# Optimization experiments

Measured on AMD Instinct MI355X. Metric: run time of the kernel, lower is better.

The kernel has to match this reference:

```python
import jax, jax.numpy as jnp
import numpy as np

B, S, D = 8, 2048, 2048
A, L = 4, 256  # audio placeholders per type per sequence, codes per placeholder
IN_IDX, OUT_IDX, PAD_ID, IGNORE = 128011, 128012, 128001, -100


def setup_inputs() -> dict:
    key = jax.random.key(0)
    k1, k2, k3, k4, k5 = jax.random.split(key, 5)
    ids = np.asarray(jax.random.randint(k1, (B, S), 0, 32000, dtype=jnp.int32)).copy()
    ids[:, np.array([100, 500, 900, 1300])] = IN_IDX
    ids[:, np.array([1700, 1800, 1900, 2000])] = OUT_IDX
    n_in = n_out = B * A
    # merged length: same for every row -> no left-pad shift, no column trim
    max_token_num = S - 2 * A + 2 * A * L  # 4088, multiple of round_to=8
    return {
        "audio_in_embed": jax.random.normal(k2, (n_in * L, D), jnp.float32),
        "audio_out_embed": jax.random.normal(k3, (n_out * L, D), jnp.float32),
        "inputs_embeds": jax.random.normal(k4, (B, S, D), jnp.float32),
        "audio_in_ids_start": jnp.arange(n_in, dtype=jnp.int32) * L,
        "audio_out_ids_start": jnp.arange(n_out, dtype=jnp.int32) * L,
        "input_ids": jnp.asarray(ids, jnp.int32),
        "attention_mask": jnp.ones((B, S), jnp.int32),
        "label_ids": jax.random.randint(k5, (B, S), 0, 32000, dtype=jnp.int32),
        "max_token_num": int(max_token_num),
        "n_in": int(n_in),
        "n_out": int(n_out),
        "n_text": int(B * S - 2 * B * A),
    }


def _codes_length(starts, total):
    # torch: concat([starts[1:]-starts[:-1], [total - starts[-1]]])
    return jnp.concatenate([starts[1:], jnp.array([total], starts.dtype)]) - starts


def _merge(audio_in_embed, audio_out_embed, inputs_embeds, audio_in_ids_start,
           audio_out_ids_start, input_ids, attention_mask, label_ids,
           max_token_num, n_in, n_out, n_text):
    Bb, Ss = input_ids.shape
    Dd = inputs_embeds.shape[-1]
    M = max_token_num

    in_mask = input_ids == IN_IDX
    out_mask = input_ids == OUT_IDX
    text_mask = ~(in_mask | out_mask)

    in_len = _codes_length(audio_in_ids_start, audio_in_embed.shape[0])
    out_len = _codes_length(audio_out_ids_start, audio_out_embed.shape[0])

    # row-major placeholder positions (matches torch.where ordering)
    bi_in, si_in = jnp.nonzero(in_mask, size=n_in)
    bi_out, si_out = jnp.nonzero(out_mask, size=n_out)
    bt, st = jnp.nonzero(text_mask, size=n_text)

    tpn = jnp.ones((Bb, Ss), jnp.int32)
    tpn = tpn.at[bi_in, si_in].set(in_len).at[bi_out, si_out].set(out_len)
    new_pos = jnp.cumsum(tpn, axis=-1) - 1
    new_pos = new_pos + (M - 1 - new_pos[:, -1])[:, None]  # left padding shift

    final_embedding = jnp.zeros((Bb, M, Dd), inputs_embeds.dtype)
    final_attention = jnp.zeros((Bb, M), attention_mask.dtype)
    final_input_ids = jnp.full((Bb, M), PAD_ID, input_ids.dtype)
    final_labels = jnp.full((Bb, M), IGNORE, label_ids.dtype)
    in_fill = jnp.zeros((Bb, M), bool)
    out_fill = jnp.zeros((Bb, M), bool)

    def fill(embed, starts, lens, b_idx, s_idx, tok_idx, FE, FI, FL, FM):
        # map each embed row -> (batch, merged column) in one gather/scatter
        r = jnp.arange(embed.shape[0], dtype=starts.dtype)
        p = jnp.searchsorted(starts, r, side='right') - 1  # placeholder id per row
        ends = new_pos[b_idx, s_idx]                        # last merged col per placeholder
        cols = ends[p] - lens[p] + 1 + (r - starts[p])
        rows = b_idx[p]
        return (FE.at[rows, cols].set(embed),
                FI.at[rows, cols].set(tok_idx),
                FL.at[rows, cols].set(IGNORE),
                FM.at[rows, cols].set(True))

    final_embedding, final_input_ids, final_labels, in_fill = fill(
        audio_in_embed, audio_in_ids_start, in_len, bi_in, si_in, IN_IDX,
        final_embedding, final_input_ids, final_labels, in_fill)
    in_discrete = in_fill
    final_embedding, final_input_ids, final_labels, out_fill = fill(
        audio_out_embed, audio_out_ids_start, out_len, bi_out, si_out, OUT_IDX,
        final_embedding, final_input_ids, final_labels, out_fill)

    tcols = new_pos[bt, st]
    final_embedding = final_embedding.at[bt, tcols].set(inputs_embeds[bt, st])
    final_labels = final_labels.at[bt, tcols].set(label_ids[bt, st])
    final_input_ids = final_input_ids.at[bt, tcols].set(input_ids[bt, st])
    final_attention = final_attention.at[bt, tcols].set(attention_mask[bt, st])
    final_attention = final_attention | (in_fill | out_fill).astype(final_attention.dtype)

    position_ids = jnp.cumsum(final_attention, axis=-1) - 1
    position_ids = jnp.where(final_attention == 0, 1, position_ids)
    return (final_embedding, final_attention, final_labels, position_ids,
            final_input_ids, in_fill, in_discrete, out_fill)


def reference(audio_in_embed, audio_out_embed, inputs_embeds, audio_in_ids_start,
              audio_out_ids_start, input_ids, attention_mask, label_ids,
              max_token_num, n_in, n_out, n_text):
    return _merge(audio_in_embed, audio_out_embed, inputs_embeds,
                  audio_in_ids_start, audio_out_ids_start, input_ids,
                  attention_mask, label_ids, max_token_num, n_in, n_out, n_text)
```

## Files before the change

### kernel.cpp

```cpp
#include <hip/hip_runtime.h>
#include <cstddef>

#define IN_IDX_C  128011
#define OUT_IDX_C 128012
#define PAD_ID_C  128001
#define IGNORE_C  (-100)

__global__ void kA_counts(const int* __restrict__ ids,
                          const int* __restrict__ pM,
                          int BM, int BS,
                          int* __restrict__ oin, int* __restrict__ oou)
{
    const int M = pM[0];
    const int B = BM / M;
    const int S = BS / B;
    __shared__ int cin[1024], cou[1024];
    for (int b = threadIdx.x; b < B; b += blockDim.x) { cin[b] = 0; cou[b] = 0; }
    __syncthreads();
    for (int i = threadIdx.x; i < BS; i += blockDim.x) {
        const int v = ids[i];
        if (v == IN_IDX_C)       atomicAdd(&cin[i / S], 1);
        else if (v == OUT_IDX_C) atomicAdd(&cou[i / S], 1);
    }
    __syncthreads();
    if (threadIdx.x == 0) {
        int oi = 0, oo = 0;
        for (int b = 0; b < B; ++b) {
            oin[b] = oi; oou[b] = oo;
            oi += cin[b]; oo += cou[b];
        }
    }
}

__global__ void kB_row(
    const int* __restrict__ ids, const int* __restrict__ attm,
    const int* __restrict__ labels,
    const int* __restrict__ in_starts, const int* __restrict__ out_starts,
    const int* __restrict__ pM, int BM, int BS,
    int inRows, int outRows, int nIn, int nOut,
    const int* __restrict__ oin, const int* __restrict__ oou,
    int* __restrict__ shiftA,
    int* __restrict__ inRowA, int* __restrict__ inCol0, int* __restrict__ inPos0,
    int* __restrict__ outRowA, int* __restrict__ outCol0, int* __restrict__ outPos0,
    int* __restrict__ map, float* __restrict__ out, int D)
{
    const int M = pM[0];
    const int B = BM / M;
    const int S = BS / B;
    const int b = blockIdx.x;
    if (b >= B) return;

    const int tid = threadIdx.x;
    const int T = blockDim.x;
    const int CH = (S + T - 1) / T;
    const int s0 = tid * CH;
    const int s1 = (s0 + CH < S) ? (s0 + CH) : S;
    const int* row = ids + (size_t)b * S;

    __shared__ int sci[256], sco[256], stp[256], sat[256];

    int ci = 0, co = 0;
    for (int s = s0; s < s1; ++s) {
        const int v = row[s];
        ci += (v == IN_IDX_C);
        co += (v == OUT_IDX_C);
    }
    sci[tid] = ci; sco[tid] = co;
    __syncthreads();
    for (int off = 1; off < T; off <<= 1) {
        int a = 0, c = 0;
        if (tid >= off) { a = sci[tid - off]; c = sco[tid - off]; }
        __syncthreads();
        sci[tid] += a; sco[tid] += c;
        __syncthreads();
    }
    const int eci = sci[tid] - ci;
    const int eco = sco[tid] - co;

    int pin = oin[b] + eci, pou = oou[b] + eco;
    int tp = 0, at = 0;
    for (int s = s0; s < s1; ++s) {
        const int v = row[s];
        if (v == IN_IDX_C) {
            const int st = in_starts[pin];
            const int en = (pin + 1 < nIn) ? in_starts[pin + 1] : inRows;
            tp += en - st; at += en - st; ++pin;
        } else if (v == OUT_IDX_C) {
            const int st = out_starts[pou];
            const int en = (pou + 1 < nOut) ? out_starts[pou + 1] : outRows;
            tp += en - st; at += en - st; ++pou;
        } else {
            tp += 1;
            at += attm[(size_t)b * S + s];
        }
    }
    stp[tid] = tp; sat[tid] = at;
    __syncthreads();
    for (int off = 1; off < T; off <<= 1) {
        int a = 0, c = 0;
        if (tid >= off) { a = stp[tid - off]; c = sat[tid - off]; }
        __syncthreads();
        stp[tid] += a; sat[tid] += c;
        __syncthreads();
    }
    const int total = stp[T - 1];
    const int shift = M - total;
    if (tid == 0) shiftA[b] = shift;

    int col  = shift + (stp[tid] - tp);
    int acum = sat[tid] - at;
    pin = oin[b] + eci; pou = oou[b] + eco;
    float* meta = out + (size_t)BM * D;
    for (int s = s0; s < s1; ++s) {
        const int v = row[s];
        if (v == IN_IDX_C) {
            const int st = in_starts[pin];
            const int en = (pin + 1 < nIn) ? in_starts[pin + 1] : inRows;
            const int len = en - st;
            inRowA[pin] = b; inCol0[pin] = col; inPos0[pin] = acum;
            col += len; acum += len; ++pin;
        } else if (v == OUT_IDX_C) {
            const int st = out_starts[pou];
            const int en = (pou + 1 < nOut) ? out_starts[pou + 1] : outRows;
            const int len = en - st;
            outRowA[pou] = b; outCol0[pou] = col; outPos0[pou] = acum;
            col += len; acum += len; ++pou;
        } else {
            const int a   = attm[(size_t)b * S + s];
            const int lab = labels[(size_t)b * S + s];
            const size_t idx = (size_t)b * M + col;
            map[idx] = s;
            meta[idx]                  = (float)a;
            meta[(size_t)BM     + idx] = (float)lab;
            meta[(size_t)BM * 2 + idx] = (a == 0) ? 1.f : (float)(acum + a - 1);
            meta[(size_t)BM * 3 + idx] = (float)v;
            meta[(size_t)BM * 4 + idx] = 0.f;
            meta[(size_t)BM * 5 + idx] = 0.f;
            meta[(size_t)BM * 6 + idx] = 0.f;
            col += 1; acum += a;
        }
    }
}

__global__ void k2_audio(
    const int* __restrict__ in_starts, const int* __restrict__ out_starts,
    const int* __restrict__ pM, int BM, int BS, int inRows, int outRows,
    int nIn, int nOut,
    const int* __restrict__ inRowA, const int* __restrict__ inCol0,
    const int* __restrict__ inPos0,
    const int* __restrict__ outRowA, const int* __restrict__ outCol0,
    const int* __restrict__ outPos0,
    int* __restrict__ map, float* __restrict__ out, int D)
{
    int r = blockIdx.x * blockDim.x + threadIdx.x;
    if (r >= inRows + outRows) return;
    const int M = pM[0];
    const int B = BM / M;
    const int S = BS / B;
    int b, col, enc, iidv, infl, outfl, pos;
    if (r < inRows) {
        int lo = 0, hi = nIn - 1;
        while (lo < hi) { int mid = (lo + hi + 1) >> 1;
                          if (in_starts[mid] <= r) lo = mid; else hi = mid - 1; }
        const int j = r - in_starts[lo];
        b = inRowA[lo]; col = inCol0[lo] + j; pos = inPos0[lo] + j;
        enc = S + r; iidv = IN_IDX_C; infl = 1; outfl = 0;
    } else {
        const int r2 = r - inRows;
        int lo = 0, hi = nOut - 1;
        while (lo < hi) { int mid = (lo + hi + 1) >> 1;
                          if (out_starts[mid] <= r2) lo = mid; else hi = mid - 1; }
        const int j = r2 - out_starts[lo];
        b = outRowA[lo]; col = outCol0[lo] + j; pos = outPos0[lo] + j;
        enc = S + inRows + r2; iidv = OUT_IDX_C; infl = 0; outfl = 1;
    }
    const size_t idx = (size_t)b * M + col;
    map[idx] = enc;
    float* meta = out + (size_t)BM * D;
    meta[idx]                  = 1.f;
    meta[(size_t)BM     + idx] = (float)IGNORE_C;
    meta[(size_t)BM * 2 + idx] = (float)pos;
    meta[(size_t)BM * 3 + idx] = (float)iidv;
    meta[(size_t)BM * 4 + idx] = (float)infl;
    meta[(size_t)BM * 5 + idx] = (float)infl;
    meta[(size_t)BM * 6 + idx] = (float)outfl;
}

__global__ void k2_pad(
    const int* __restrict__ pM, int BM,
    const int* __restrict__ shiftA,
    int* __restrict__ map, float* __restrict__ out, int D)
{
    int i = blockIdx.x * blockDim.x + threadIdx.x;
    if (i >= BM) return;
    const int M = pM[0];
    const int b = i / M, m = i - b * M;
    if (m >= shiftA[b]) return;
    map[i] = -1;
    float* meta = out + (size_t)BM * D;
    meta[i]                  = 0.f;
    meta[(size_t)BM     + i] = (float)IGNORE_C;
    meta[(size_t)BM * 2 + i] = 1.f;
    meta[(size_t)BM * 3 + i] = (float)PAD_ID_C;
    meta[(size_t)BM * 4 + i] = 0.f;
    meta[(size_t)BM * 5 + i] = 0.f;
    meta[(size_t)BM * 6 + i] = 0.f;
}

__global__ void k4_copy(
    const float* __restrict__ audio_in, const float* __restrict__ audio_out,
    const float* __restrict__ inputs_embeds, const int* __restrict__ pM,
    int BM, int BS, int inRows, int D,
    const int* __restrict__ map, float* __restrict__ out)
{
    const int bm = blockIdx.x;
    const int v = map[bm];
    float4* dst = (float4*)(out + (size_t)bm * D);
    const int nq = D >> 2;
    if (v < 0) {
        const float4 z = make_float4(0.f, 0.f, 0.f, 0.f);
        for (int i = threadIdx.x; i < nq; i += blockDim.x) dst[i] = z;
        return;
    }
    const int M = pM[0];
    const int B = BM / M;
    const int S = BS / B;
    const float* src;
    if (v < S) {
        const int b = bm / M;
        src = inputs_embeds + ((size_t)b * S + v) * (size_t)D;
    } else if (v < S + inRows) {
        src = audio_in + (size_t)(v - S) * D;
    } else {
        src = audio_out + (size_t)(v - S - inRows) * D;
    }
    const float4* s4 = (const float4*)src;
    for (int i = threadIdx.x; i < nq; i += blockDim.x) dst[i] = s4[i];
}

extern "C" void kernel_launch(void* const* d_in, const int* in_sizes, int n_inputs,
                              void* d_out, int out_size, void* d_ws, size_t ws_size,
                              hipStream_t stream) {
    (void)n_inputs; (void)ws_size;
    const float* audio_in      = (const float*)d_in[0];
    const float* audio_out     = (const float*)d_in[1];
    const float* inputs_embeds = (const float*)d_in[2];
    const int* in_starts  = (const int*)d_in[3];
    const int* out_starts = (const int*)d_in[4];
    const int* ids        = (const int*)d_in[5];
    const int* attm       = (const int*)d_in[6];
    const int* labels     = (const int*)d_in[7];
    const int* pM         = (const int*)d_in[8];

    const int nIn     = in_sizes[3];
    const int nOut    = in_sizes[4];
    const int BS      = in_sizes[5];
    const int D       = in_sizes[2] / BS;
    const int inRows  = in_sizes[0] / D;
    const int outRows = in_sizes[1] / D;
    const int BM      = out_size / (D + 7);

    int* wsI     = (int*)d_ws;
    int* map     = wsI;
    int* shiftA  = map + BM;
    int* oin     = shiftA + 2048;
    int* oou     = oin + 2048;
    int* inRowA  = oou + 2048;
    int* inCol0  = inRowA + nIn;
    int* inPos0  = inCol0 + nIn;
    int* outRowA = inPos0 + nIn;
    int* outCol0 = outRowA + nOut;
    int* outPos0 = outCol0 + nOut;

    float* out = (float*)d_out;

    hipLaunchKernelGGL(kA_counts, dim3(1), dim3(1024), 0, stream,
        ids, pM, BM, BS, oin, oou);

    hipLaunchKernelGGL(kB_row, dim3(2048), dim3(256), 0, stream,
        ids, attm, labels, in_starts, out_starts, pM, BM, BS,
        inRows, outRows, nIn, nOut, oin, oou,
        shiftA, inRowA, inCol0, inPos0, outRowA, outCol0, outPos0,
        map, out, D);

    const int ar = inRows + outRows;
    hipLaunchKernelGGL(k2_audio, dim3((ar + 255) / 256), dim3(256), 0, stream,
        in_starts, out_starts, pM, BM, BS, inRows, outRows, nIn, nOut,
        inRowA, inCol0, inPos0, outRowA, outCol0, outPos0, map, out, D);

    hipLaunchKernelGGL(k2_pad, dim3((BM + 255) / 256), dim3(256), 0, stream,
        pM, BM, shiftA, map, out, D);

    hipLaunchKernelGGL(k4_copy, dim3(BM), dim3(256), 0, stream,
        audio_in, audio_out, inputs_embeds, pM, BM, BS, inRows, D, map, out);
}
```

Measured before the change: 478.8 us.

## Fuse planning kernels into one per-row kernel with wave scans and nontemporal copy

Merges the count, row-plan, audio-metadata and pad kernels into a single per-row kernel. Each block recomputes its prefix of placeholder counts, replaces the shared-memory Hillis-Steele scans with wave-shuffle scans on packed 16-bit pairs, and keeps placeholder segments in shared memory to write the audio and pad metadata directly. The copy kernel now uses nontemporal stores. This cuts four launches down to two and removes the binary search and the global scratch arrays. The trade-offs are a redundant prefix scan over earlier rows in every block, 16-bit packing limits on the counts, and a cap of 256 placeholders per row.

```diff
diff --git a/kernel.cpp b/kernel.cpp
--- a/kernel.cpp
+++ b/kernel.cpp
@@ -6,42 +6,48 @@
 #define PAD_ID_C  128001
 #define IGNORE_C  (-100)
 
-__global__ void kA_counts(const int* __restrict__ ids,
-                          const int* __restrict__ pM,
-                          int BM, int BS,
-                          int* __restrict__ oin, int* __restrict__ oou)
+#define TB   1024
+#define NW   (TB / 64)
+#define MAXP 256
+
+typedef float f32x4 __attribute__((ext_vector_type(4)));
+
+__device__ __forceinline__ unsigned block_scan(unsigned x, unsigned* wp,
+                                               unsigned* tot)
 {
-    const int M = pM[0];
-    const int B = BM / M;
-    const int S = BS / B;
-    __shared__ int cin[1024], cou[1024];
-    for (int b = threadIdx.x; b < B; b += blockDim.x) { cin[b] = 0; cou[b] = 0; }
-    __syncthreads();
-    for (int i = threadIdx.x; i < BS; i += blockDim.x) {
-        const int v = ids[i];
-        if (v == IN_IDX_C)       atomicAdd(&cin[i / S], 1);
-        else if (v == OUT_IDX_C) atomicAdd(&cou[i / S], 1);
-    }
-    __syncthreads();
-    if (threadIdx.x == 0) {
-        int oi = 0, oo = 0;
-        for (int b = 0; b < B; ++b) {
-            oin[b] = oi; oou[b] = oo;
-            oi += cin[b]; oo += cou[b];
-        }
-    }
-}
-
-__global__ void kB_row(
+    const int tid  = threadIdx.x;
+    const int lane = tid & 63;
+    const int w    = tid >> 6;
+    unsigned v = x;
+    #pragma unroll
+    for (int off = 1; off < 64; off <<= 1) {
+        unsigned y = (unsigned)__shfl_up((int)v, off);
+        if (lane >= off) v += y;
+    }
+    __syncthreads();
+    if (lane == 63) wp[w] = v;
+    __syncthreads();
+    if (w == 0) {
+        unsigned pv = (lane < NW) ? wp[lane] : 0u;
+        #pragma unroll
+        for (int off = 1; off < NW; off <<= 1) {
+            unsigned y = (unsigned)__shfl_up((int)pv, off);
+            if (lane >= off) pv += y;
+        }
+        if (lane < NW) wp[lane] = pv;
+    }
+    __syncthreads();
+    const unsigned base = (w > 0) ? wp[w - 1] : 0u;
+    *tot = wp[NW - 1];
+    return v + base;
+}
+
+__global__ __launch_bounds__(TB) void k_plan(
     const int* __restrict__ ids, const int* __restrict__ attm,
     const int* __restrict__ labels,
     const int* __restrict__ in_starts, const int* __restrict__ out_starts,
     const int* __restrict__ pM, int BM, int BS,
     int inRows, int outRows, int nIn, int nOut,
-    const int* __restrict__ oin, const int* __restrict__ oou,
-    int* __restrict__ shiftA,
-    int* __restrict__ inRowA, int* __restrict__ inCol0, int* __restrict__ inPos0,
-    int* __restrict__ outRowA, int* __restrict__ outCol0, int* __restrict__ outPos0,
     int* __restrict__ map, float* __restrict__ out, int D)
 {
     const int M = pM[0];
@@ -51,13 +57,26 @@
     if (b >= B) return;
 
     const int tid = threadIdx.x;
-    const int T = blockDim.x;
-    const int CH = (S + T - 1) / T;
-    const int s0 = tid * CH;
-    const int s1 = (s0 + CH < S) ? (s0 + CH) : S;
+    const int CH = (S + TB - 1) / TB;
+    int s0 = tid * CH; if (s0 > S) s0 = S;
+    int s1 = s0 + CH;  if (s1 > S) s1 = S;
     const int* row = ids + (size_t)b * S;
 
-    __shared__ int sci[256], sco[256], stp[256], sat[256];
+    __shared__ unsigned wp[NW];
+    __shared__ int pInCol0[MAXP], pInPos0[MAXP], pInStart[MAXP], pInLen[MAXP];
+    __shared__ int pOutCol0[MAXP], pOutPos0[MAXP], pOutStart[MAXP], pOutLen[MAXP];
+
+    int cip = 0, cop = 0;
+    const int P = b * S;
+    for (int i = tid; i < P; i += TB) {
+        const int v = ids[i];
+        cip += (v == IN_IDX_C);
+        cop += (v == OUT_IDX_C);
+    }
+    unsigned tot0;
+    block_scan(((unsigned)cip << 16) | (unsigned)cop, wp, &tot0);
+    const int oinB = (int)(tot0 >> 16);
+    const int oouB = (int)(tot0 & 0xffffu);
 
     int ci = 0, co = 0;
     for (int s = s0; s < s1; ++s) {
@@ -65,19 +84,13 @@
         ci += (v == IN_IDX_C);
         co += (v == OUT_IDX_C);
     }
-    sci[tid] = ci; sco[tid] = co;
-    __syncthreads();
-    for (int off = 1; off < T; off <<= 1) {
-        int a = 0, c = 0;
-        if (tid >= off) { a = sci[tid - off]; c = sco[tid - off]; }
-        __syncthreads();
-        sci[tid] += a; sco[tid] += c;
-        __syncthreads();
-    }
-    const int eci = sci[tid] - ci;
-    const int eco = sco[tid] - co;
-
-    int pin = oin[b] + eci, pou = oou[b] + eco;
+    unsigned tot1;
+    const unsigned pk1 = ((unsigned)ci << 16) | (unsigned)co;
+    const unsigned ex1 = block_scan(pk1, wp, &tot1) - pk1;
+    const int eci = (int)(ex1 >> 16), eco = (int)(ex1 & 0xffffu);
+    const int rowIn = (int)(tot1 >> 16), rowOut = (int)(tot1 & 0xffffu);
+
+    int pin = oinB + eci, pou = oouB + eco;
     int tp = 0, at = 0;
     for (int s = s0; s < s1; ++s) {
         const int v = row[s];
@@ -94,22 +107,15 @@
             at += attm[(size_t)b * S + s];
         }
     }
-    stp[tid] = tp; sat[tid] = at;
-    __syncthreads();
-    for (int off = 1; off < T; off <<= 1) {
-        int a = 0, c = 0;
-        if (tid >= off) { a = stp[tid - off]; c = sat[tid - off]; }
-        __syncthreads();
-        stp[tid] += a; sat[tid] += c;
-        __syncthreads();
-    }
-    const int total = stp[T - 1];
+    unsigned tot2;
+    const unsigned pk2 = ((unsigned)tp << 16) | (unsigned)at;
+    const unsigned ex2 = block_scan(pk2, wp, &tot2) - pk2;
+    const int total = (int)(tot2 >> 16);
     const int shift = M - total;
-    if (tid == 0) shiftA[b] = shift;
-
-    int col  = shift + (stp[tid] - tp);
-    int acum = sat[tid] - at;
-    pin = oin[b] + eci; pou = oou[b] + eco;
+
+    int col  = shift + (int)(ex2 >> 16);
+    int acum = (int)(ex2 & 0xffffu);
+    pin = oinB + eci; pou = oouB + eco;
     float* meta = out + (size_t)BM * D;
     for (int s = s0; s < s1; ++s) {
         const int v = row[s];
@@ -117,13 +123,21 @@
             const int st = in_starts[pin];
             const int en = (pin + 1 < nIn) ? in_starts[pin + 1] : inRows;
             const int len = en - st;
-            inRowA[pin] = b; inCol0[pin] = col; inPos0[pin] = acum;
+            const int li = pin - oinB;
+            if (li < MAXP) {
+                pInCol0[li] = col; pInPos0[li] = acum;
+                pInStart[li] = st; pInLen[li] = len;
+            }
             col += len; acum += len; ++pin;
         } else if (v == OUT_IDX_C) {
             const int st = out_starts[pou];
             const int en = (pou + 1 < nOut) ? out_starts[pou + 1] : outRows;
             const int len = en - st;
-            outRowA[pou] = b; outCol0[pou] = col; outPos0[pou] = acum;
+            const int li = pou - oouB;
+            if (li < MAXP) {
+                pOutCol0[li] = col; pOutPos0[li] = acum;
+                pOutStart[li] = st; pOutLen[li] = len;
+            }
             col += len; acum += len; ++pou;
         } else {
             const int a   = attm[(size_t)b * S + s];
@@ -140,74 +154,54 @@
             col += 1; acum += a;
         }
     }
-}
-
-__global__ void k2_audio(
-    const int* __restrict__ in_starts, const int* __restrict__ out_starts,
-    const int* __restrict__ pM, int BM, int BS, int inRows, int outRows,
-    int nIn, int nOut,
-    const int* __restrict__ inRowA, const int* __restrict__ inCol0,
-    const int* __restrict__ inPos0,
-    const int* __restrict__ outRowA, const int* __restrict__ outCol0,
-    const int* __restrict__ outPos0,
-    int* __restrict__ map, float* __restrict__ out, int D)
-{
-    int r = blockIdx.x * blockDim.x + threadIdx.x;
-    if (r >= inRows + outRows) return;
-    const int M = pM[0];
-    const int B = BM / M;
-    const int S = BS / B;
-    int b, col, enc, iidv, infl, outfl, pos;
-    if (r < inRows) {
-        int lo = 0, hi = nIn - 1;
-        while (lo < hi) { int mid = (lo + hi + 1) >> 1;
-                          if (in_starts[mid] <= r) lo = mid; else hi = mid - 1; }
-        const int j = r - in_starts[lo];
-        b = inRowA[lo]; col = inCol0[lo] + j; pos = inPos0[lo] + j;
-        enc = S + r; iidv = IN_IDX_C; infl = 1; outfl = 0;
-    } else {
-        const int r2 = r - inRows;
-        int lo = 0, hi = nOut - 1;
-        while (lo < hi) { int mid = (lo + hi + 1) >> 1;
-                          if (out_starts[mid] <= r2) lo = mid; else hi = mid - 1; }
-        const int j = r2 - out_starts[lo];
-        b = outRowA[lo]; col = outCol0[lo] + j; pos = outPos0[lo] + j;
-        enc = S + inRows + r2; iidv = OUT_IDX_C; infl = 0; outfl = 1;
-    }
-    const size_t idx = (size_t)b * M + col;
-    map[idx] = enc;
-    float* meta = out + (size_t)BM * D;
-    meta[idx]                  = 1.f;
-    meta[(size_t)BM     + idx] = (float)IGNORE_C;
-    meta[(size_t)BM * 2 + idx] = (float)pos;
-    meta[(size_t)BM * 3 + idx] = (float)iidv;
-    meta[(size_t)BM * 4 + idx] = (float)infl;
-    meta[(size_t)BM * 5 + idx] = (float)infl;
-    meta[(size_t)BM * 6 + idx] = (float)outfl;
-}
-
-__global__ void k2_pad(
-    const int* __restrict__ pM, int BM,
-    const int* __restrict__ shiftA,
-    int* __restrict__ map, float* __restrict__ out, int D)
-{
-    int i = blockIdx.x * blockDim.x + threadIdx.x;
-    if (i >= BM) return;
-    const int M = pM[0];
-    const int b = i / M, m = i - b * M;
-    if (m >= shiftA[b]) return;
-    map[i] = -1;
-    float* meta = out + (size_t)BM * D;
-    meta[i]                  = 0.f;
-    meta[(size_t)BM     + i] = (float)IGNORE_C;
-    meta[(size_t)BM * 2 + i] = 1.f;
-    meta[(size_t)BM * 3 + i] = (float)PAD_ID_C;
-    meta[(size_t)BM * 4 + i] = 0.f;
-    meta[(size_t)BM * 5 + i] = 0.f;
-    meta[(size_t)BM * 6 + i] = 0.f;
-}
-
-__global__ void k4_copy(
+    __syncthreads();
+
+    const int nI = rowIn < MAXP ? rowIn : MAXP;
+    for (int k = 0; k < nI; ++k) {
+        const int c0 = pInCol0[k], p0 = pInPos0[k];
+        const int st = pInStart[k], len = pInLen[k];
+        for (int j = tid; j < len; j += TB) {
+            const size_t idx = (size_t)b * M + c0 + j;
+            map[idx] = S + st + j;
+            meta[idx]                  = 1.f;
+            meta[(size_t)BM     + idx] = (float)IGNORE_C;
+            meta[(size_t)BM * 2 + idx] = (float)(p0 + j);
+            meta[(size_t)BM * 3 + idx] = (float)IN_IDX_C;
+            meta[(size_t)BM * 4 + idx] = 1.f;
+            meta[(size_t)BM * 5 + idx] = 1.f;
+            meta[(size_t)BM * 6 + idx] = 0.f;
+        }
+    }
+    const int nO = rowOut < MAXP ? rowOut : MAXP;
+    for (int k = 0; k < nO; ++k) {
+        const int c0 = pOutCol0[k], p0 = pOutPos0[k];
+        const int st = pOutStart[k], len = pOutLen[k];
+        for (int j = tid; j < len; j += TB) {
+            const size_t idx = (size_t)b * M + c0 + j;
+            map[idx] = S + inRows + st + j;
+            meta[idx]                  = 1.f;
+            meta[(size_t)BM     + idx] = (float)IGNORE_C;
+            meta[(size_t)BM * 2 + idx] = (float)(p0 + j);
+            meta[(size_t)BM * 3 + idx] = (float)OUT_IDX_C;
+            meta[(size_t)BM * 4 + idx] = 0.f;
+            meta[(size_t)BM * 5 + idx] = 0.f;
+            meta[(size_t)BM * 6 + idx] = 1.f;
+        }
+    }
+    for (int m = tid; m < shift; m += TB) {
+        const size_t idx = (size_t)b * M + m;
+        map[idx] = -1;
+        meta[idx]                  = 0.f;
+        meta[(size_t)BM     + idx] = (float)IGNORE_C;
+        meta[(size_t)BM * 2 + idx] = 1.f;
+        meta[(size_t)BM * 3 + idx] = (float)PAD_ID_C;
+        meta[(size_t)BM * 4 + idx] = 0.f;
+        meta[(size_t)BM * 5 + idx] = 0.f;
+        meta[(size_t)BM * 6 + idx] = 0.f;
+    }
+}
+
+__global__ __launch_bounds__(256) void k_copy(
     const float* __restrict__ audio_in, const float* __restrict__ audio_out,
     const float* __restrict__ inputs_embeds, const int* __restrict__ pM,
     int BM, int BS, int inRows, int D,
@@ -215,11 +209,12 @@
 {
     const int bm = blockIdx.x;
     const int v = map[bm];
-    float4* dst = (float4*)(out + (size_t)bm * D);
+    f32x4* dst = (f32x4*)(out + (size_t)bm * D);
     const int nq = D >> 2;
     if (v < 0) {
-        const float4 z = make_float4(0.f, 0.f, 0.f, 0.f);
-        for (int i = threadIdx.x; i < nq; i += blockDim.x) dst[i] = z;
+        const f32x4 z = {0.f, 0.f, 0.f, 0.f};
+        for (int i = threadIdx.x; i < nq; i += blockDim.x)
+            __builtin_nontemporal_store(z, &dst[i]);
         return;
     }
     const int M = pM[0];
@@ -234,8 +229,9 @@
     } else {
         src = audio_out + (size_t)(v - S - inRows) * D;
     }
-    const float4* s4 = (const float4*)src;
-    for (int i = threadIdx.x; i < nq; i += blockDim.x) dst[i] = s4[i];
+    const f32x4* s4 = (const f32x4*)src;
+    for (int i = threadIdx.x; i < nq; i += blockDim.x)
+        __builtin_nontemporal_store(s4[i], &dst[i]);
 }
 
 extern "C" void kernel_launch(void* const* d_in, const int* in_sizes, int n_inputs,
@@ -260,37 +256,13 @@
     const int outRows = in_sizes[1] / D;
     const int BM      = out_size / (D + 7);
 
-    int* wsI     = (int*)d_ws;
-    int* map     = wsI;
-    int* shiftA  = map + BM;
-    int* oin     = shiftA + 2048;
-    int* oou     = oin + 2048;
-    int* inRowA  = oou + 2048;
-    int* inCol0  = inRowA + nIn;
-    int* inPos0  = inCol0 + nIn;
-    int* outRowA = inPos0 + nIn;
-    int* outCol0 = outRowA + nOut;
-    int* outPos0 = outCol0 + nOut;
-
+    int* map = (int*)d_ws;
     float* out = (float*)d_out;
 
-    hipLaunchKernelGGL(kA_counts, dim3(1), dim3(1024), 0, stream,
-        ids, pM, BM, BS, oin, oou);
-
-    hipLaunchKernelGGL(kB_row, dim3(2048), dim3(256), 0, stream,
+    hipLaunchKernelGGL(k_plan, dim3(2048), dim3(TB), 0, stream,
         ids, attm, labels, in_starts, out_starts, pM, BM, BS,
-        inRows, outRows, nIn, nOut, oin, oou,
-        shiftA, inRowA, inCol0, inPos0, outRowA, outCol0, outPos0,
-        map, out, D);
-
-    const int ar = inRows + outRows;
-    hipLaunchKernelGGL(k2_audio, dim3((ar + 255) / 256), dim3(256), 0, stream,
-        in_starts, out_starts, pM, BM, BS, inRows, outRows, nIn, nOut,
-        inRowA, inCol0, inPos0, outRowA, outCol0, outPos0, map, out, D);
-
-    hipLaunchKernelGGL(k2_pad, dim3((BM + 255) / 256), dim3(256), 0, stream,
-        pM, BM, shiftA, map, out, D);
-
-    hipLaunchKernelGGL(k4_copy, dim3(BM), dim3(256), 0, stream,
+        inRows, outRows, nIn, nOut, map, out, D);
+
+    hipLaunchKernelGGL(k_copy, dim3(BM), dim3(256), 0, stream,
         audio_in, audio_out, inputs_embeds, pM, BM, BS, inRows, D, map, out);
 }
```

Result: no change. 470.9 us (-1.7%).
